# Performance work log

Hardware: AMD Instinct MI355X
Metric: run time of the kernel (lower is better)

## Reference

```python
import jax, jax.numpy as jnp
import numpy as np

SCALE = 500.0  # config.scale
RADIUS = 1.1   # config.radius


def setup_inputs() -> dict:
    key = jax.random.key(0)
    k1, k2, k3 = jax.random.split(key, 3)
    N, D, T, R, B = 65536, 3, 64, 64, 64
    x = jax.random.normal(k1, (N, D), dtype=jnp.float32)
    directions = jax.random.normal(k2, (D, T), dtype=jnp.float32)
    directions = directions / jnp.linalg.norm(directions, axis=0, keepdims=True)  # unit directions
    lin = jnp.linspace(-RADIUS, RADIUS, R, dtype=jnp.float32)
    batch = jnp.sort(jax.random.randint(k3, (N,), 0, B)).astype(jnp.int64)
    return {"x": x, "directions": directions, "lin": lin, "batch": batch, "dim_size": B}


def reference(x, directions, lin, batch, dim_size):
    # nh: height of each point along each direction. [N, T]
    nh = x @ directions
    N, T = nh.shape
    R = lin.shape[0]
    # Sigmoid-smoothed indicator of (height <= threshold). [N, R, T]
    ecc = jax.nn.sigmoid(SCALE * (lin[None, :, None] - nh[:, None, :]))
    # Scatter-accumulate per point cloud. [B, R, T]
    ect = jax.ops.segment_sum(
        ecc.reshape(N, R * T), batch, num_segments=dim_size,
        indices_are_sorted=True,
    ).reshape(dim_size, R, T)
    return ect
```

## Files before the change

### kernel.cpp

```cpp
#include <hip/hip_runtime.h>


#define T_DIRS   64
#define R_STEPS  64
#define NROWS    65
#define N_BATCH  64
#define TSPLIT   16
#define TQW      4
#define PSW      16
#define THREADS  512
#define NWAVES   8
#define WIN      768

#define RADIUS_F 1.1f
#define STEP_F   (2.0f * RADIUS_F / (R_STEPS - 1))
#define INV_STEP (1.0f / STEP_F)
#define OFF_F    (RADIUS_F * INV_STEP)
#define MEXP     (-500.0f * STEP_F * 1.4426950408889634f)
#define FIXP     512.0f
#define INV_FIXP (1.0f / 512.0f)
#define CNT_ONE  (1u << 20)
#define SI_MASK  0xFFFFFu

__global__ __launch_bounds__(THREADS) void ect_kernel(
    const float* __restrict__ x,
    const float* __restrict__ dirs,
    const int*   __restrict__ batch,
    float* __restrict__ out,
    int N)
{
    __shared__ unsigned s_a[NROWS * TQW];
    __shared__ int      s_lo, s_hi;

    const int tid  = threadIdx.x;
    const int b    = blockIdx.x >> 4;
    const int q    = blockIdx.x & (TSPLIT - 1);
    const int lane = tid & 63;
    const int w    = tid >> 6;
    const int ps   = lane >> 2;
    const int tq   = lane & (TQW - 1);
    const int tg   = q * TQW + tq;

    for (int i = tid; i < NROWS * TQW; i += THREADS) s_a[i] = 0u;
    if (tid == 0) {
        s_lo = (b == 0) ? 0 : -1;
        s_hi = (b == N_BATCH - 1) ? N : -1;
    }

    const float d0 = dirs[tg];
    const float d1 = dirs[T_DIRS + tg];
    const float d2 = dirs[2 * T_DIRS + tg];
    __syncthreads();

    {
        const int seg = N >> 6;
        if (b != 0) {
            int c0 = b * seg;
            int a0 = max(0, c0 - WIN), a1 = min(N, c0 + WIN);
            for (int j = a0 + tid; j < a1; j += THREADS) {
                int v  = batch[j];
                int vp = (j == 0) ? -1 : batch[j - 1];
                if (v >= b && vp < b) s_lo = j;
            }
        }
        if (b != N_BATCH - 1) {
            int c1 = (b + 1) * seg;
            int b0 = max(0, c1 - WIN), b1 = min(N, c1 + WIN);
            for (int j = b0 + tid; j < b1; j += THREADS) {
                int v  = batch[j];
                int vp = (j == 0) ? -1 : batch[j - 1];
                if (v > b && vp <= b) s_hi = j;
            }
        }
    }
    __syncthreads();

    if (s_lo < 0 || s_hi < 0) {
        for (int j = tid; j < N; j += THREADS) {
            int v  = batch[j];
            int vp = (j == 0) ? -1 : batch[j - 1];
            if (v >= b && vp < b)  s_lo = j;
            if (v >  b && vp <= b) s_hi = j;
        }
        __syncthreads();
    }
    const int lo  = (s_lo < 0) ? N : s_lo;
    const int hi  = (s_hi < 0) ? N : s_hi;
    const int len = hi - lo;
    const float* xb = x + (size_t)lo * 3;

    for (int p = w * PSW + ps; p < len; p += NWAVES * PSW) {
        float x0 = xb[p * 3 + 0];
        float x1 = xb[p * 3 + 1];
        float x2 = xb[p * 3 + 2];
        float nh  = fmaf(x2, d2, fmaf(x1, d1, x0 * d0));
        float u   = fmaf(nh, INV_STEP, OFF_F);
        float r0f = rintf(u);
        float dd  = r0f - u;
        float e   = __builtin_amdgcn_exp2f(dd * MEXP);
        float s   = __builtin_amdgcn_rcpf(1.0f + e);
        unsigned si = (unsigned)fmaf(s, FIXP, 0.5f);
        int j1 = (int)r0f + 1;
        if (j1 <= R_STEPS) {
            j1 = max(j1, 0);
            atomicAdd(&s_a[j1 * TQW + tq], CNT_ONE | si);
        }
    }
    __syncthreads();
    if (w != 0) return;

    uint4 rowv = *(const uint4*)&s_a[lane * TQW];
    uint4 r64  = *(const uint4*)&s_a[R_STEPS * TQW];

    unsigned c0 = rowv.x >> 20, c1 = rowv.y >> 20,
             c2 = rowv.z >> 20, c3 = rowv.w >> 20;
    unsigned s0 = rowv.x & SI_MASK, s1 = rowv.y & SI_MASK,
             s2 = rowv.z & SI_MASK, s3 = rowv.w & SI_MASK;

    unsigned n0 = __shfl_down(s0, 1, 64), n1 = __shfl_down(s1, 1, 64),
             n2 = __shfl_down(s2, 1, 64), n3 = __shfl_down(s3, 1, 64);
    if (lane == 63) {
        n0 = r64.x & SI_MASK; n1 = r64.y & SI_MASK;
        n2 = r64.z & SI_MASK; n3 = r64.w & SI_MASK;
    }

#pragma unroll
    for (int d = 1; d < 64; d <<= 1) {
        unsigned u0 = __shfl_up(c0, d, 64), u1 = __shfl_up(c1, d, 64),
                 u2 = __shfl_up(c2, d, 64), u3 = __shfl_up(c3, d, 64);
        if (lane >= d) { c0 += u0; c1 += u1; c2 += u2; c3 += u3; }
    }

    float4 o;
    o.x = (float)c0 + (float)n0 * INV_FIXP;
    o.y = (float)c1 + (float)n1 * INV_FIXP;
    o.z = (float)c2 + (float)n2 * INV_FIXP;
    o.w = (float)c3 + (float)n3 * INV_FIXP;
    *(float4*)&out[((size_t)b << 12) | (lane << 6) | (q * TQW)] = o;
}

extern "C" void kernel_launch(void* const* d_in, const int* in_sizes, int n_in,
                              void* d_out, int out_size, void* d_ws, size_t ws_size,
                              hipStream_t stream) {
    const float* x     = (const float*)d_in[0];
    const float* dirs  = (const float*)d_in[1];
    const int*   batch = (const int*)d_in[3];
    float* out = (float*)d_out;
    const int N = in_sizes[3];

    ect_kernel<<<dim3(N_BATCH * TSPLIT), dim3(THREADS), 0, stream>>>(
        x, dirs, batch, out, N);
}
```

Baseline: 12.12 us.

## Vectorize boundary search and point loads, reorder block-to-batch mapping

The block index mapping is swapped so consecutive blocks cover different batches instead of direction quarters. The boundary search now splits the block into two halves, one per boundary, with each thread loading 8 batch entries via two vector loads and checking 7 transitions. Point coordinates are read with an unaligned 4-float load except for the final point, to avoid reading out of bounds. This cuts the number of load instructions and loop iterations, at the cost of unaligned vector accesses and some redundant bytes read.

```diff
diff --git a/kernel.cpp b/kernel.cpp
--- a/kernel.cpp
+++ b/kernel.cpp
@@ -22,6 +22,9 @@
 #define CNT_ONE  (1u << 20)
 #define SI_MASK  0xFFFFFu
 
+typedef int   int4u __attribute__((ext_vector_type(4), aligned(4)));
+typedef float f4u   __attribute__((ext_vector_type(4), aligned(4)));
+
 __global__ __launch_bounds__(THREADS) void ect_kernel(
     const float* __restrict__ x,
     const float* __restrict__ dirs,
@@ -33,8 +36,8 @@
     __shared__ int      s_lo, s_hi;
 
     const int tid  = threadIdx.x;
-    const int b    = blockIdx.x >> 4;
-    const int q    = blockIdx.x & (TSPLIT - 1);
+    const int b    = blockIdx.x & 63;
+    const int q    = blockIdx.x >> 6;
     const int lane = tid & 63;
     const int w    = tid >> 6;
     const int ps   = lane >> 2;
@@ -54,22 +57,22 @@
 
     {
         const int seg = N >> 6;
-        if (b != 0) {
-            int c0 = b * seg;
-            int a0 = max(0, c0 - WIN), a1 = min(N, c0 + WIN);
-            for (int j = a0 + tid; j < a1; j += THREADS) {
-                int v  = batch[j];
-                int vp = (j == 0) ? -1 : batch[j - 1];
-                if (v >= b && vp < b) s_lo = j;
-            }
-        }
-        if (b != N_BATCH - 1) {
-            int c1 = (b + 1) * seg;
-            int b0 = max(0, c1 - WIN), b1 = min(N, c1 + WIN);
-            for (int j = b0 + tid; j < b1; j += THREADS) {
-                int v  = batch[j];
-                int vp = (j == 0) ? -1 : batch[j - 1];
-                if (v > b && vp <= b) s_hi = j;
+        const bool isLo = (tid < 256);
+        const int  t2   = isLo ? tid : (tid - 256);
+        const int  c    = (isLo ? b : (b + 1)) * seg;
+        const bool run  = isLo ? (b != 0) : (b != N_BATCH - 1);
+        if (run) {
+            int base = c - WIN - 1 + t2 * 7;
+            int4u ea = *(const int4u*)&batch[base];
+            int4u eb = *(const int4u*)&batch[base + 4];
+            int e[8] = {ea.x, ea.y, ea.z, ea.w, eb.x, eb.y, eb.z, eb.w};
+#pragma unroll
+            for (int i = 0; i < 7; ++i) {
+                int j = base + 1 + i;
+                if (j < c + WIN) {
+                    if (isLo) { if (e[i+1] >= b && e[i] <  b) s_lo = j; }
+                    else      { if (e[i+1] >  b && e[i] <= b) s_hi = j; }
+                }
             }
         }
     }
@@ -88,11 +91,16 @@
     const int hi  = (s_hi < 0) ? N : s_hi;
     const int len = hi - lo;
     const float* xb = x + (size_t)lo * 3;
+    const int lastN = N - 1 - lo;
 
     for (int p = w * PSW + ps; p < len; p += NWAVES * PSW) {
-        float x0 = xb[p * 3 + 0];
-        float x1 = xb[p * 3 + 1];
-        float x2 = xb[p * 3 + 2];
+        float x0, x1, x2;
+        if (p != lastN) {
+            f4u v = *(const f4u*)(xb + (size_t)p * 3);
+            x0 = v.x; x1 = v.y; x2 = v.z;
+        } else {
+            x0 = xb[p * 3]; x1 = xb[p * 3 + 1]; x2 = xb[p * 3 + 2];
+        }
         float nh  = fmaf(x2, d2, fmaf(x1, d1, x0 * d0));
         float u   = fmaf(nh, INV_STEP, OFF_F);
         float r0f = rintf(u);
```

Result: slower. 17.30 us (+42.7%).
